# Performance work log

Measured on AMD Instinct MI355X. Metric: run time of the kernel, lower is better.

The kernel has to match this reference:

```python
import jax, jax.numpy as jnp
import numpy as np

N, IN_DIM = 50000, 1024
E = 100000
NUM_REL = 40
HEADS, OUT_DIM = 4, 200
HID = HEADS * OUT_DIM  # 800
B = 8192
NEG_SLOPE = 0.2


def setup_inputs() -> dict:
    key = jax.random.key(0)
    ks = jax.random.split(key, 12)
    node_emb = jax.random.normal(ks[0], (N, IN_DIM), dtype=jnp.float32)
    # RelGAT learnable params
    W = jax.random.normal(ks[1], (IN_DIM, HID), dtype=jnp.float32) * (1.0 / np.sqrt(IN_DIM))
    bias = jnp.zeros((HID,), dtype=jnp.float32)
    a_src = jax.random.normal(ks[2], (HEADS, OUT_DIM), dtype=jnp.float32) * 0.1
    a_dst = jax.random.normal(ks[3], (HEADS, OUT_DIM), dtype=jnp.float32) * 0.1
    a_rel = jax.random.normal(ks[4], (HEADS, OUT_DIM), dtype=jnp.float32) * 0.1
    rel_feat = jax.random.normal(ks[5], (NUM_REL, HID), dtype=jnp.float32) * 0.1
    # DistMult scorer relation embeddings
    rel_emb = jax.random.normal(ks[6], (NUM_REL, HID), dtype=jnp.float32) * 0.1
    # Graph structure (constants)
    edge_index = jax.random.randint(ks[7], (2, E), 0, N, dtype=jnp.int64)
    edge_type = jax.random.randint(ks[8], (E,), 0, NUM_REL, dtype=jnp.int64)
    # Triple batch
    src_ids = jax.random.randint(ks[9], (B,), 0, N, dtype=jnp.int64)
    rel_ids = jax.random.randint(ks[10], (B,), 0, NUM_REL, dtype=jnp.int64)
    dst_ids = jax.random.randint(ks[11], (B,), 0, N, dtype=jnp.int64)
    return dict(node_emb=node_emb, W=W, bias=bias, a_src=a_src, a_dst=a_dst,
                a_rel=a_rel, rel_feat=rel_feat, rel_emb=rel_emb,
                edge_index=edge_index, edge_type=edge_type,
                src_ids=src_ids, rel_ids=rel_ids, dst_ids=dst_ids)


def _rel_gat(node_emb, W, bias, a_src, a_dst, a_rel, rel_feat, edge_index, edge_type):
    src, dst = edge_index[0], edge_index[1]
    h = (node_emb @ W).reshape(N, HEADS, OUT_DIM)          # [N,H,D]
    hs = h[src]                                            # [E,H,D] gather
    hd = h[dst]                                            # [E,H,D] gather
    r = rel_feat[edge_type].reshape(E, HEADS, OUT_DIM)     # [E,H,D]
    # relation-conditioned attention logits per head
    logits = (jnp.einsum('ehd,hd->eh', hs, a_src)
              + jnp.einsum('ehd,hd->eh', hd, a_dst)
              + jnp.einsum('ehd,hd->eh', r, a_rel))        # [E,H]
    logits = jax.nn.leaky_relu(logits, NEG_SLOPE)
    # segment softmax over incoming edges of each destination node
    seg_max = jax.ops.segment_max(logits, dst, num_segments=N)   # [N,H]
    e = jnp.exp(logits - seg_max[dst])                           # [E,H]
    denom = jax.ops.segment_sum(e, dst, num_segments=N)          # [N,H]
    alpha = e / denom[dst]                                       # [E,H]
    # weighted scatter-aggregate of source messages
    out = jax.ops.segment_sum(alpha[:, :, None] * hs, dst, num_segments=N)  # [N,H,D]
    return out.reshape(N, HID) + bias                            # dropout: eval mode (identity)


def reference(node_emb, W, bias, a_src, a_dst, a_rel, rel_feat, rel_emb,
              edge_index, edge_type, src_ids, rel_ids, dst_ids):
    refined = _rel_gat(node_emb, W, bias, a_src, a_dst, a_rel, rel_feat,
                       edge_index, edge_type)                # [N, HID]
    src_vec = refined[src_ids]                               # [B, HID]
    dst_vec = refined[dst_ids]                               # [B, HID]
    # DistMult: sum(s * r * d)
    scores = jnp.sum(src_vec * rel_emb[rel_ids] * dst_vec, axis=-1)  # [B]
    return scores
```

## Files before the change

kernel.cpp:

```cpp
#include <hip/hip_runtime.h>
#include <hip/hip_bf16.h>
#include <math.h>

#define NN 50000
#define IN_DIM 1024
#define EE 100000
#define NUM_REL 40
#define HEADS 4
#define OUT_D 200
#define HID 800
#define BB 8192
#define SLOT_CAP 16384
#define SRC_CAP 50176
#define WT_COLS 896

typedef __attribute__((ext_vector_type(8))) short short8;
typedef __attribute__((ext_vector_type(4))) float f32x4;

__device__ inline unsigned short f2bf(float f) {
    unsigned int u = __float_as_uint(f);
    u += 0x7FFF + ((u >> 16) & 1);
    return (unsigned short)(u >> 16);
}
__device__ inline float bf2f(unsigned short s) {
    return __uint_as_float(((unsigned int)s) << 16);
}
__device__ inline void gl2lds16(const unsigned short* g, unsigned short* l) {
    __builtin_amdgcn_global_load_lds(
        (const __attribute__((address_space(1))) void*)g,
        (__attribute__((address_space(3))) void*)l, 16, 0, 0);
}

__device__ inline int wave_compact(bool won, int* ctr) {
    unsigned long long m = __ballot(won);
    if (!m) return -1;
    int lane = threadIdx.x & 63;
    int leader = __ffsll((long long)m) - 1;
    int base = 0;
    if (lane == leader) base = atomicAdd(ctr, __popcll(m));
    base = __shfl(base, leader, 64);
    return won ? base + __popcll(m & ((1ull << lane) - 1)) : -1;
}

#define INIT_BLOCKS 196
__global__ __launch_bounds__(256) void k_init_wa(int* slot_of_node, int* xrow_of_node,
                                                 int* deg, int* counters,
                                                 const float* W, const float* a_src,
                                                 const float* a_dst, const float* a_rel,
                                                 const float* rel_feat, float* Wa, float* prel) {
    int b = blockIdx.x;
    if (b < INIT_BLOCKS) {
        int i = b * 256 + threadIdx.x;
        if (i < NN) { slot_of_node[i] = -1; xrow_of_node[i] = -1; }
        if (i < SLOT_CAP) deg[i] = 0;
        if (i < 8) counters[i] = 0;
        return;
    }
    int wid = (b - INIT_BLOCKS) * 4 + (threadIdx.x >> 6);
    int lane = threadIdx.x & 63;
    if (wid >= IN_DIM * 8 + NUM_REL * HEADS) return;
    float acc = 0.f;
    int d = lane * 4;
    if (d < OUT_D) {
        const float* row;
        const float* a;
        if (wid < IN_DIM * 8) {
            int k = wid >> 3, c = wid & 7;
            int h = c & 3;
            row = W + (size_t)k * HID + h * OUT_D;
            a = ((c < 4) ? a_src : a_dst) + h * OUT_D;
        } else {
            int j = wid - IN_DIM * 8;
            int r = j >> 2, h = j & 3;
            row = rel_feat + (size_t)r * HID + h * OUT_D;
            a = a_rel + h * OUT_D;
        }
        float4 wv = *(const float4*)(row + d);
        float4 av = *(const float4*)(a + d);
        acc = wv.x * av.x + wv.y * av.y + wv.z * av.z + wv.w * av.w;
    }
    for (int off = 32; off; off >>= 1) acc += __shfl_down(acc, off, 64);
    if (lane == 0) {
        if (wid < IN_DIM * 8) Wa[wid] = acc;
        else prel[wid - IN_DIM * 8] = acc;
    }
}

__global__ void k_build_slots(const int* src_ids, const int* dst_ids,
                              int* slot_of_node, int* counters, int* scorelist) {
    int i = blockIdx.x * 256 + threadIdx.x;
    bool valid = i < 2 * BB;
    int n = 0;
    bool won = false;
    if (valid) {
        n = (i < BB) ? src_ids[i] : dst_ids[i - BB];
        if (slot_of_node[n] == -1)
            won = (atomicCAS(&slot_of_node[n], -1, -2) == -1);
    }
    int s = wave_compact(won, &counters[0]);
    if (won) {
        slot_of_node[n] = s;
        scorelist[s] = n;
    }
}

__global__ void k_edge0(const int* ei, const int* slot_of_node,
                        int* xrow_of_node, int* counters, int* rows, int* deg) {
    int e = blockIdx.x * 256 + threadIdx.x;
    bool valid = e < EE;
    int slot = -1, sn = 0;
    if (valid) {
        int dn = ei[EE + e];
        slot = slot_of_node[dn];
    }
    bool surv = valid && slot >= 0;
    bool won = false;
    if (surv) {
        sn = ei[e];
        if (xrow_of_node[sn] == -1)
            won = (atomicCAS(&xrow_of_node[sn], -1, -2) == -1);
    }
    int t = wave_compact(won, &counters[1]);
    if (won) {
        rows[t] = sn;
        xrow_of_node[sn] = t;
    }
    if (surv) atomicAdd(&deg[slot], 1);
}

__global__ __launch_bounds__(256) void k_tail_scan(const int* scorelist, int* xrow_of_node,
                                                   int* counters, int* rows,
                                                   const int* deg, int* base, int* cursor) {
    int t = threadIdx.x;
    if (blockIdx.x == 0) {
        __shared__ int pref[257];
        int s = 0;
        const int4* dv = (const int4*)(deg + t * (SLOT_CAP / 256));
        for (int i = 0; i < SLOT_CAP / 256 / 4; ++i) {
            int4 v = dv[i];
            s += v.x + v.y + v.z + v.w;
        }
        pref[t + 1] = s;
        if (t == 0) pref[0] = 0;
        __syncthreads();
        if (t == 0)
            for (int i = 1; i <= 256; ++i) pref[i] += pref[i - 1];
        __syncthreads();
        int r = pref[t];
        for (int i = 0; i < SLOT_CAP / 256; ++i) {
            int idx = t * (SLOT_CAP / 256) + i;
            base[idx] = r;
            cursor[idx] = r;
            r += deg[idx];
        }
        return;
    }
    int i = (blockIdx.x - 1) * 256 + t;
    bool valid = i < counters[0];
    int n = 0;
    bool won = false;
    if (valid) {
        n = scorelist[i];
        won = (xrow_of_node[n] < 0);
    }
    int tt = wave_compact(won, &counters[3]);
    if (won) {
        int xr = counters[1] + tt;
        xrow_of_node[n] = xr;
        rows[xr] = n;
    }
}

#define WT_BLOCKS 224
#define GATHER_BLOCKS 3584
__global__ __launch_bounds__(256) void k_gather_wt(const float* x, const int* rows,
                                                   const int* counters, unsigned short* xg,
                                                   const float* W, const float* Wa,
                                                   unsigned short* Wt) {
    int t = threadIdx.x;
    if (blockIdx.x < WT_BLOCKS) {
        __shared__ float tile[64][65];
        int b = blockIdx.x;
        int k0 = (b & 15) * 64, c0 = (b >> 4) * 64;
        {
            int kk = t >> 2, cc = (t & 3) * 16;
            for (int i = 0; i < 16; ++i) {
                int c = c0 + cc + i;
                float v = 0.f;
                if (c < HID) v = W[(size_t)(k0 + kk) * HID + c];
                else if (c < HID + 8) v = Wa[(size_t)(k0 + kk) * 8 + (c - HID)];
                tile[cc + i][kk] = v;
            }
        }
        __syncthreads();
        {
            int cc = t >> 2, kk = (t & 3) * 16;
            unsigned short o[16];
            for (int i = 0; i < 16; ++i) o[i] = f2bf(tile[cc][kk + i]);
            *(short8*)(Wt + (size_t)(c0 + cc) * IN_DIM + k0 + kk) = *(short8*)o;
            *(short8*)(Wt + (size_t)(c0 + cc) * IN_DIM + k0 + kk + 8) = *(short8*)(o + 8);
        }
        return;
    }
    int nneed = counters[1] + counters[3];
    int lim = nneed * 128;
    for (int gid = (blockIdx.x - WT_BLOCKS) * 256 + t; gid < lim;
         gid += GATHER_BLOCKS * 256) {
        int row = gid >> 7;
        int j = (gid & 127) * 8;
        int node = rows[row];
        const float* src = x + (size_t)node * IN_DIM + j;
        float4 a = *(const float4*)(src);
        float4 b = *(const float4*)(src + 4);
        unsigned short o[8] = {f2bf(a.x), f2bf(a.y), f2bf(a.z), f2bf(a.w),
                               f2bf(b.x), f2bf(b.y), f2bf(b.z), f2bf(b.w)};
        *(short8*)(xg + (size_t)row * IN_DIM + j) = *(short8*)o;
    }
}

#define GBM 256
#define GBN 128
#define GBK 64

#define STAGE(AS, BS, K0) do {                                          \
    gl2lds16(aP0 + (K0),      (AS) + (size_t)(0 * 512 + t) * 8);        \
    gl2lds16(aP1 + (K0),      (AS) + (size_t)(1 * 512 + t) * 8);        \
    gl2lds16(aP0 + (K0) + 32, (AS) + (size_t)(2 * 512 + t) * 8);        \
    gl2lds16(aP1 + (K0) + 32, (AS) + (size_t)(3 * 512 + t) * 8);        \
    gl2lds16(bP  + (K0),      (BS) + (size_t)(0 * 512 + t) * 8);        \
    gl2lds16(bP  + (K0) + 32, (BS) + (size_t)(1 * 512 + t) * 8);        \
} while (0)

#define COMPUTE(AS, BS) do {                                            \
    _Pragma("unroll")                                                   \
    for (int s = 0; s < 2; ++s) {                                       \
        short8 af[4], bf4[4];                                           \
        _Pragma("unroll")                                               \
        for (int i = 0; i < 4; ++i)                                     \
            af[i] = *(const short8*)&(AS)[(size_t)(s * 1024 + (gm + i) * 64 + lane) * 8]; \
        _Pragma("unroll")                                               \
        for (int j = 0; j < 4; ++j)                                     \
            bf4[j] = *(const short8*)&(BS)[(size_t)(s * 512 + (gn + j) * 64 + lane) * 8]; \
        __builtin_amdgcn_s_setprio(1);                                  \
        _Pragma("unroll")                                               \
        for (int i = 0; i < 4; ++i)                                     \
            _Pragma("unroll")                                           \
            for (int j = 0; j < 4; ++j)                                 \
                acc[i][j] = __builtin_amdgcn_mfma_f32_16x16x32_bf16(af[i], bf4[j], acc[i][j], 0, 0, 0); \
        __builtin_amdgcn_s_setprio(0);                                  \
    }                                                                   \
} while (0)

#define GATE6 asm volatile("s_waitcnt vmcnt(6)\n\ts_barrier" ::: "memory")
#define GATE0 asm volatile("s_waitcnt vmcnt(0)\n\ts_barrier" ::: "memory")
#define BARX  asm volatile("s_barrier" ::: "memory")

__global__ __launch_bounds__(512) void k_hgemm(const unsigned short* xg, const unsigned short* Wt,
                                               const int* counters, unsigned short* h_src,
                                               float* sS, float* sD) {
    int nsrc = counters[1];
    int nneed = nsrc + counters[3];
    int lin = blockIdx.x + 7 * blockIdx.y;
    int g = lin / 56, r = lin % 56;
    int rowb = g * 8 + (r & 7);
    int colb = r >> 3;
    int col0 = colb * GBN;
    int row0 = rowb * GBM;
    int rowlim = (col0 == 768) ? nneed : nsrc;
    if (row0 >= rowlim) return;
    __shared__ unsigned short As0[GBM * GBK];
    __shared__ unsigned short As1[GBM * GBK];
    __shared__ unsigned short Bs0[GBN * GBK];
    __shared__ unsigned short Bs1[GBN * GBK];
    int t = threadIdx.x;
    int rb = ((t >> 6) << 4) + (t & 15);
    int kb = ((t >> 4) & 3) << 3;
    const unsigned short* aP0 = xg + (size_t)(row0 + rb) * IN_DIM + kb;
    const unsigned short* aP1 = aP0 + (size_t)128 * IN_DIM;
    const unsigned short* bP  = Wt + (size_t)(col0 + rb) * IN_DIM + kb;
    int w = t >> 6, lane = t & 63;
    int gm = (w >> 1) * 4, gn = (w & 1) * 4;
    int wr = (w >> 1) * 64, wc = (w & 1) * 64;
    int fm = lane & 15, fq = lane >> 4;
    f32x4 acc[4][4] = {};
    STAGE(As0, Bs0, 0);
#pragma unroll 1
    for (int kk = 0; kk < 16; kk += 2) {
        STAGE(As1, Bs1, (kk + 1) * 64);
        GATE6;
        COMPUTE(As0, Bs0);
        BARX;
        if (kk < 14) {
            STAGE(As0, Bs0, (kk + 2) * 64);
            GATE6;
        } else {
            GATE0;
        }
        COMPUTE(As1, Bs1);
        BARX;
    }
#pragma unroll
    for (int i = 0; i < 4; ++i) {
#pragma unroll
        for (int j = 0; j < 4; ++j) {
            int gcol = col0 + wc + j * 16 + fm;
            if (gcol >= HID + 8) continue;
#pragma unroll
            for (int rr = 0; rr < 4; ++rr) {
                int grow = row0 + wr + i * 16 + fq * 4 + rr;
                float v = acc[i][j][rr];
                if (gcol < HID) {
                    if (grow < nsrc) h_src[(size_t)grow * HID + gcol] = f2bf(v);
                } else if (grow < nneed) {
                    int c = gcol - HID;
                    if (c < 4) sS[grow * 4 + c] = v;
                    else sD[grow * 4 + (c - 4)] = v;
                }
            }
        }
    }
}

__global__ void k_place(const int* ei, const int* etype, const int* slot_of_node,
                        const int* xrow_of_node, int* cursor,
                        const float* sS, const float* sD, const float* prel,
                        float* clogit, int* tlist) {
    int e = blockIdx.x * 256 + threadIdx.x;
    if (e >= EE) return;
    int dn = ei[EE + e];
    int slot = slot_of_node[dn];
    if (slot < 0) return;
    int sn = ei[e];
    int r = etype[e];
    int xs = xrow_of_node[sn];
    int xd = xrow_of_node[dn];
    int pos = atomicAdd(&cursor[slot], 1);
    tlist[pos] = xs;
    float4 lg;
    float* lp = (float*)&lg;
#pragma unroll
    for (int h = 0; h < 4; ++h) {
        float v = sS[xs * 4 + h] + sD[xd * 4 + h] + prel[r * 4 + h];
        lp[h] = v > 0.f ? v : 0.2f * v;
    }
    *(float4*)&clogit[(size_t)pos * 4] = lg;
}

__global__ __launch_bounds__(256) void k_aggregate(const int* counters, const int* base,
                                                   const int* deg, const int* tlist,
                                                   const float* clogit,
                                                   const unsigned short* h_src, const float* bias,
                                                   float* refined) {
    int b = blockIdx.x;
    if (b >= counters[0]) return;
    int beg = base[b], d = deg[b];
    __shared__ float m4[4], den4[4];
    __shared__ float alpha[64][4];
    __shared__ int tsl[64];
    int t = threadIdx.x;
    if (t < 4) {
        float m = -3e38f;
        for (int j = 0; j < d; ++j)
            m = fmaxf(m, clogit[(size_t)(beg + j) * 4 + t]);
        float s = 0.f;
        for (int j = 0; j < d; ++j)
            s += expf(clogit[(size_t)(beg + j) * 4 + t] - m);
        m4[t] = m;
        den4[t] = s;
    }
    __syncthreads();
    int head = t / 50;
    float4 acc = {0.f, 0.f, 0.f, 0.f};
    for (int j0 = 0; j0 < d; j0 += 64) {
        int nc = min(64, d - j0);
        if (t < nc * 4) {
            int j = t >> 2, h = t & 3;
            alpha[j][h] = expf(clogit[(size_t)(beg + j0 + j) * 4 + h] - m4[h]) / den4[h];
            if (h == 0) tsl[j] = tlist[beg + j0 + j];
        }
        __syncthreads();
        if (t < 200) {
            for (int j = 0; j < nc; ++j) {
                float a = alpha[j][head];
                ushort4 hv = *(const ushort4*)(h_src + (size_t)tsl[j] * HID + t * 4);
                acc.x += a * bf2f(hv.x);
                acc.y += a * bf2f(hv.y);
                acc.z += a * bf2f(hv.z);
                acc.w += a * bf2f(hv.w);
            }
        }
        __syncthreads();
    }
    if (t < 200) {
        float4 bv = *(const float4*)(bias + t * 4);
        float4 o = {acc.x + bv.x, acc.y + bv.y, acc.z + bv.z, acc.w + bv.w};
        *(float4*)(refined + (size_t)b * HID + t * 4) = o;
    }
}

__global__ __launch_bounds__(256) void k_score(const int* src_ids, const int* rel_ids,
                                               const int* dst_ids, const int* slot_of_node,
                                               const float* rel_emb, const float* refined,
                                               float* out) {
    int gid = blockIdx.x * 256 + threadIdx.x;
    int b = gid >> 6;
    int lane = threadIdx.x & 63;
    if (b >= BB) return;
    int ss = slot_of_node[src_ids[b]];
    int ds = slot_of_node[dst_ids[b]];
    int r = rel_ids[b];
    const float* sv = refined + (size_t)ss * HID;
    const float* dv = refined + (size_t)ds * HID;
    const float* rv = rel_emb + (size_t)r * HID;
    float acc = 0.f;
    for (int c4 = lane; c4 < 200; c4 += 64) {
        float4 s = *(const float4*)(sv + c4 * 4);
        float4 dq = *(const float4*)(dv + c4 * 4);
        float4 rr = *(const float4*)(rv + c4 * 4);
        acc += s.x * rr.x * dq.x + s.y * rr.y * dq.y + s.z * rr.z * dq.z + s.w * rr.w * dq.w;
    }
    for (int off = 32; off; off >>= 1) acc += __shfl_down(acc, off, 64);
    if (lane == 0) out[b] = acc;
}

extern "C" void kernel_launch(void* const* d_in, const int* in_sizes, int n_in,
                              void* d_out, int out_size, void* d_ws, size_t ws_size,
                              hipStream_t stream) {
    const float* node_emb = (const float*)d_in[0];
    const float* W        = (const float*)d_in[1];
    const float* bias     = (const float*)d_in[2];
    const float* a_src    = (const float*)d_in[3];
    const float* a_dst    = (const float*)d_in[4];
    const float* a_rel    = (const float*)d_in[5];
    const float* rel_feat = (const float*)d_in[6];
    const float* rel_emb  = (const float*)d_in[7];
    const int* edge_index = (const int*)d_in[8];
    const int* edge_type  = (const int*)d_in[9];
    const int* src_ids    = (const int*)d_in[10];
    const int* rel_ids    = (const int*)d_in[11];
    const int* dst_ids    = (const int*)d_in[12];
    float* out = (float*)d_out;

    char* w = (char*)d_ws;
    auto alloc = [&](size_t bytes) -> void* {
        void* p = (void*)w;
        w += (bytes + 255) & ~(size_t)255;
        return p;
    };
    int* slot_of_node = (int*)alloc((size_t)NN * 4);
    int* xrow_of_node = (int*)alloc((size_t)NN * 4);
    int* scorelist    = (int*)alloc((size_t)SLOT_CAP * 4);
    int* rows         = (int*)alloc((size_t)NN * 4);
    int* counters     = (int*)alloc(256);
    int* deg          = (int*)alloc((size_t)SLOT_CAP * 4);
    int* base         = (int*)alloc((size_t)SLOT_CAP * 4);
    int* cursor       = (int*)alloc((size_t)SLOT_CAP * 4);
    int* tlist        = (int*)alloc((size_t)EE * 4);
    float* clogit = (float*)alloc((size_t)EE * 4 * 4);
    float* sS     = (float*)alloc((size_t)SRC_CAP * 4 * 4);
    float* sD     = (float*)alloc((size_t)SRC_CAP * 4 * 4);
    float* Wa     = (float*)alloc((size_t)IN_DIM * 8 * 4);
    float* prel   = (float*)alloc((size_t)NUM_REL * 4 * 4);
    unsigned short* xg    = (unsigned short*)alloc((size_t)SRC_CAP * IN_DIM * 2);
    unsigned short* Wt    = (unsigned short*)alloc((size_t)WT_COLS * IN_DIM * 2);
    unsigned short* h_src = (unsigned short*)alloc((size_t)SRC_CAP * HID * 2);
    float* refined = (float*)alloc((size_t)SLOT_CAP * HID * 4);

    int wa_blocks = (IN_DIM * 8 + NUM_REL * HEADS + 3) / 4;
    k_init_wa<<<INIT_BLOCKS + wa_blocks, 256, 0, stream>>>(
        slot_of_node, xrow_of_node, deg, counters,
        W, a_src, a_dst, a_rel, rel_feat, Wa, prel);
    k_build_slots<<<(2 * BB + 255) / 256, 256, 0, stream>>>(src_ids, dst_ids, slot_of_node,
                                                            counters, scorelist);
    k_edge0<<<(EE + 255) / 256, 256, 0, stream>>>(edge_index, slot_of_node,
                                                  xrow_of_node, counters, rows, deg);
    k_tail_scan<<<1 + SLOT_CAP / 256, 256, 0, stream>>>(scorelist, xrow_of_node, counters,
                                                        rows, deg, base, cursor);
    k_gather_wt<<<WT_BLOCKS + GATHER_BLOCKS, 256, 0, stream>>>(
        node_emb, rows, counters, xg, W, Wa, Wt);
    dim3 ggrid(7, 200);
    k_hgemm<<<ggrid, 512, 0, stream>>>(xg, Wt, counters, h_src, sS, sD);
    k_place<<<(EE + 255) / 256, 256, 0, stream>>>(edge_index, edge_type, slot_of_node,
                                                  xrow_of_node, cursor, sS, sD, prel,
                                                  clogit, tlist);
    k_aggregate<<<SLOT_CAP, 256, 0, stream>>>(counters, base, deg, tlist,
                                              clogit, h_src, bias, refined);
    k_score<<<(BB * 64 + 255) / 256, 256, 0, stream>>>(src_ids, rel_ids, dst_ids,
                                                       slot_of_node, rel_emb, refined, out);
}
```

Baseline: 504.1 us.

## Fuse row gather and bf16 conversion into GEMM A-tile loading

```diff
diff --git a/kernel.cpp b/kernel.cpp
--- a/kernel.cpp
+++ b/kernel.cpp
@@ -128,9 +128,11 @@
     if (surv) atomicAdd(&deg[slot], 1);
 }
 
-__global__ __launch_bounds__(256) void k_tail_scan(const int* scorelist, int* xrow_of_node,
-                                                   int* counters, int* rows,
-                                                   const int* deg, int* base, int* cursor) {
+__global__ __launch_bounds__(256) void k_tail_scan_wt(const int* scorelist, int* xrow_of_node,
+                                                      int* counters, int* rows,
+                                                      const int* deg, int* base, int* cursor,
+                                                      const float* W, const float* Wa,
+                                                      unsigned short* Wt) {
     int t = threadIdx.x;
     if (blockIdx.x == 0) {
         __shared__ int pref[257];
@@ -155,80 +157,78 @@
         }
         return;
     }
-    int i = (blockIdx.x - 1) * 256 + t;
-    bool valid = i < counters[0];
-    int n = 0;
-    bool won = false;
-    if (valid) {
-        n = scorelist[i];
-        won = (xrow_of_node[n] < 0);
-    }
-    int tt = wave_compact(won, &counters[3]);
-    if (won) {
-        int xr = counters[1] + tt;
-        xrow_of_node[n] = xr;
-        rows[xr] = n;
-    }
-}
-
-#define WT_BLOCKS 224
-#define GATHER_BLOCKS 3584
-__global__ __launch_bounds__(256) void k_gather_wt(const float* x, const int* rows,
-                                                   const int* counters, unsigned short* xg,
-                                                   const float* W, const float* Wa,
-                                                   unsigned short* Wt) {
-    int t = threadIdx.x;
-    if (blockIdx.x < WT_BLOCKS) {
-        __shared__ float tile[64][65];
-        int b = blockIdx.x;
-        int k0 = (b & 15) * 64, c0 = (b >> 4) * 64;
-        {
-            int kk = t >> 2, cc = (t & 3) * 16;
-            for (int i = 0; i < 16; ++i) {
-                int c = c0 + cc + i;
-                float v = 0.f;
-                if (c < HID) v = W[(size_t)(k0 + kk) * HID + c];
-                else if (c < HID + 8) v = Wa[(size_t)(k0 + kk) * 8 + (c - HID)];
-                tile[cc + i][kk] = v;
-            }
-        }
-        __syncthreads();
-        {
-            int cc = t >> 2, kk = (t & 3) * 16;
-            unsigned short o[16];
-            for (int i = 0; i < 16; ++i) o[i] = f2bf(tile[cc][kk + i]);
-            *(short8*)(Wt + (size_t)(c0 + cc) * IN_DIM + k0 + kk) = *(short8*)o;
-            *(short8*)(Wt + (size_t)(c0 + cc) * IN_DIM + k0 + kk + 8) = *(short8*)(o + 8);
+    if (blockIdx.x <= 64) {
+        int i = (blockIdx.x - 1) * 256 + t;
+        bool valid = i < counters[0];
+        int n = 0;
+        bool won = false;
+        if (valid) {
+            n = scorelist[i];
+            won = (xrow_of_node[n] < 0);
+        }
+        int tt = wave_compact(won, &counters[3]);
+        if (won) {
+            int xr = counters[1] + tt;
+            xrow_of_node[n] = xr;
+            rows[xr] = n;
         }
         return;
     }
-    int nneed = counters[1] + counters[3];
-    int lim = nneed * 128;
-    for (int gid = (blockIdx.x - WT_BLOCKS) * 256 + t; gid < lim;
-         gid += GATHER_BLOCKS * 256) {
-        int row = gid >> 7;
-        int j = (gid & 127) * 8;
-        int node = rows[row];
-        const float* src = x + (size_t)node * IN_DIM + j;
-        float4 a = *(const float4*)(src);
-        float4 b = *(const float4*)(src + 4);
-        unsigned short o[8] = {f2bf(a.x), f2bf(a.y), f2bf(a.z), f2bf(a.w),
-                               f2bf(b.x), f2bf(b.y), f2bf(b.z), f2bf(b.w)};
-        *(short8*)(xg + (size_t)row * IN_DIM + j) = *(short8*)o;
-    }
-}
-
-#define GBM 256
+    __shared__ float tile[64][65];
+    int b = blockIdx.x - 65;
+    int k0 = (b & 15) * 64, c0 = (b >> 4) * 64;
+    {
+        int kk = t >> 2, cc = (t & 3) * 16;
+        for (int i = 0; i < 16; ++i) {
+            int c = c0 + cc + i;
+            float v = 0.f;
+            if (c < HID) v = W[(size_t)(k0 + kk) * HID + c];
+            else if (c < HID + 8) v = Wa[(size_t)(k0 + kk) * 8 + (c - HID)];
+            tile[cc + i][kk] = v;
+        }
+    }
+    __syncthreads();
+    {
+        int cc = t >> 2, kk = (t & 3) * 16;
+        unsigned short o[16];
+        for (int i = 0; i < 16; ++i) o[i] = f2bf(tile[cc][kk + i]);
+        *(short8*)(Wt + (size_t)(c0 + cc) * IN_DIM + k0 + kk) = *(short8*)o;
+        *(short8*)(Wt + (size_t)(c0 + cc) * IN_DIM + k0 + kk + 8) = *(short8*)(o + 8);
+    }
+}
+
+#define GBM 128
 #define GBN 128
 #define GBK 64
 
-#define STAGE(AS, BS, K0) do {                                          \
-    gl2lds16(aP0 + (K0),      (AS) + (size_t)(0 * 512 + t) * 8);        \
-    gl2lds16(aP1 + (K0),      (AS) + (size_t)(1 * 512 + t) * 8);        \
-    gl2lds16(aP0 + (K0) + 32, (AS) + (size_t)(2 * 512 + t) * 8);        \
-    gl2lds16(aP1 + (K0) + 32, (AS) + (size_t)(3 * 512 + t) * 8);        \
-    gl2lds16(bP  + (K0),      (BS) + (size_t)(0 * 512 + t) * 8);        \
-    gl2lds16(bP  + (K0) + 32, (BS) + (size_t)(1 * 512 + t) * 8);        \
+#define ALOAD(K0) do {                                                  \
+    av[0] = *(const float4*)(ax0 + (K0));                               \
+    av[1] = *(const float4*)(ax0 + (K0) + 4);                           \
+    av[2] = *(const float4*)(ax1 + (K0));                               \
+    av[3] = *(const float4*)(ax1 + (K0) + 4);                           \
+    av[4] = *(const float4*)(ax0 + (K0) + 32);                          \
+    av[5] = *(const float4*)(ax0 + (K0) + 36);                          \
+    av[6] = *(const float4*)(ax1 + (K0) + 32);                          \
+    av[7] = *(const float4*)(ax1 + (K0) + 36);                          \
+} while (0)
+
+#define AWRITE(AS) do {                                                 \
+    unsigned short o[8];                                                \
+    _Pragma("unroll")                                                   \
+    for (int q = 0; q < 4; ++q) {                                       \
+        o[0] = f2bf(av[2*q].x); o[1] = f2bf(av[2*q].y);                 \
+        o[2] = f2bf(av[2*q].z); o[3] = f2bf(av[2*q].w);                 \
+        o[4] = f2bf(av[2*q+1].x); o[5] = f2bf(av[2*q+1].y);             \
+        o[6] = f2bf(av[2*q+1].z); o[7] = f2bf(av[2*q+1].w);             \
+        *(short8*)&(AS)[(size_t)(q * 256 + t) * 8] = *(short8*)o;       \
+    }                                                                   \
+} while (0)
+
+#define BSTAGE(BS, K0) do {                                             \
+    gl2lds16(bP0 + (K0),      (BS) + (size_t)(0 * 256 + t) * 8);        \
+    gl2lds16(bP1 + (K0),      (BS) + (size_t)(1 * 256 + t) * 8);        \
+    gl2lds16(bP0 + (K0) + 32, (BS) + (size_t)(2 * 256 + t) * 8);        \
+    gl2lds16(bP1 + (K0) + 32, (BS) + (size_t)(3 * 256 + t) * 8);        \
 } while (0)
 
 #define COMPUTE(AS, BS) do {                                            \
@@ -237,10 +237,10 @@
         short8 af[4], bf4[4];                                           \
         _Pragma("unroll")                                               \
         for (int i = 0; i < 4; ++i)                                     \
-            af[i] = *(const short8*)&(AS)[(size_t)(s * 1024 + (gm + i) * 64 + lane) * 8]; \
+            af[i] = *(const short8*)&(AS)[(size_t)(s * 512 + (ga + i) * 64 + lane) * 8]; \
         _Pragma("unroll")                                               \
         for (int j = 0; j < 4; ++j)                                     \
-            bf4[j] = *(const short8*)&(BS)[(size_t)(s * 512 + (gn + j) * 64 + lane) * 8]; \
+            bf4[j] = *(const short8*)&(BS)[(size_t)(s * 512 + (gb + j) * 64 + lane) * 8]; \
         __builtin_amdgcn_s_setprio(1);                                  \
         _Pragma("unroll")                                               \
         for (int i = 0; i < 4; ++i)                                     \
@@ -251,11 +251,12 @@
     }                                                                   \
 } while (0)
 
-#define GATE6 asm volatile("s_waitcnt vmcnt(6)\n\ts_barrier" ::: "memory")
-#define GATE0 asm volatile("s_waitcnt vmcnt(0)\n\ts_barrier" ::: "memory")
-#define BARX  asm volatile("s_barrier" ::: "memory")
-
-__global__ __launch_bounds__(512) void k_hgemm(const unsigned short* xg, const unsigned short* Wt,
+#define WAIT_A  asm volatile("s_waitcnt vmcnt(4)" ::: "memory")
+#define PUBLISH asm volatile("s_waitcnt vmcnt(0) lgkmcnt(0)" ::: "memory")
+#define BARX    asm volatile("s_barrier" ::: "memory")
+
+__global__ __launch_bounds__(256) void k_hgemm(const float* x, const int* rows,
+                                               const unsigned short* Wt,
                                                const int* counters, unsigned short* h_src,
                                                float* sS, float* sD) {
     int nsrc = counters[1];
@@ -273,31 +274,49 @@
     __shared__ unsigned short Bs0[GBN * GBK];
     __shared__ unsigned short Bs1[GBN * GBK];
     int t = threadIdx.x;
-    int rb = ((t >> 6) << 4) + (t & 15);
-    int kb = ((t >> 4) & 3) << 3;
-    const unsigned short* aP0 = xg + (size_t)(row0 + rb) * IN_DIM + kb;
-    const unsigned short* aP1 = aP0 + (size_t)128 * IN_DIM;
-    const unsigned short* bP  = Wt + (size_t)(col0 + rb) * IN_DIM + kb;
+    int crow = ((t >> 6) << 4) + (t & 15);
+    int coff = ((t >> 4) & 3) << 3;
+    int lim = nneed - 1;
+    int n0 = rows[min(row0 + crow, lim)];
+    int n1 = rows[min(row0 + crow + 64, lim)];
+    const float* ax0 = x + (size_t)n0 * IN_DIM + coff;
+    const float* ax1 = x + (size_t)n1 * IN_DIM + coff;
+    const unsigned short* bP0 = Wt + (size_t)(col0 + crow) * IN_DIM + coff;
+    const unsigned short* bP1 = bP0 + (size_t)64 * IN_DIM;
     int w = t >> 6, lane = t & 63;
-    int gm = (w >> 1) * 4, gn = (w & 1) * 4;
+    int ga = (w >> 1) * 4, gb = (w & 1) * 4;
     int wr = (w >> 1) * 64, wc = (w & 1) * 64;
     int fm = lane & 15, fq = lane >> 4;
+    float4 av[8];
     f32x4 acc[4][4] = {};
-    STAGE(As0, Bs0, 0);
+    ALOAD(0);
+    BSTAGE(Bs0, 0);
+    WAIT_A;
+    AWRITE(As0);
+    PUBLISH;
+    BARX;
 #pragma unroll 1
     for (int kk = 0; kk < 16; kk += 2) {
-        STAGE(As1, Bs1, (kk + 1) * 64);
-        GATE6;
+        ALOAD((kk + 1) * 64);
+        BSTAGE(Bs1, (kk + 1) * 64);
         COMPUTE(As0, Bs0);
         BARX;
+        WAIT_A;
+        AWRITE(As1);
+        PUBLISH;
+        BARX;
         if (kk < 14) {
-            STAGE(As0, Bs0, (kk + 2) * 64);
-            GATE6;
-        } else {
-            GATE0;
+            ALOAD((kk + 2) * 64);
+            BSTAGE(Bs0, (kk + 2) * 64);
         }
         COMPUTE(As1, Bs1);
         BARX;
+        if (kk < 14) {
+            WAIT_A;
+            AWRITE(As0);
+            PUBLISH;
+            BARX;
+        }
     }
 #pragma unroll
     for (int i = 0; i < 4; ++i) {
@@ -461,7 +480,6 @@
     float* sD     = (float*)alloc((size_t)SRC_CAP * 4 * 4);
     float* Wa     = (float*)alloc((size_t)IN_DIM * 8 * 4);
     float* prel   = (float*)alloc((size_t)NUM_REL * 4 * 4);
-    unsigned short* xg    = (unsigned short*)alloc((size_t)SRC_CAP * IN_DIM * 2);
     unsigned short* Wt    = (unsigned short*)alloc((size_t)WT_COLS * IN_DIM * 2);
     unsigned short* h_src = (unsigned short*)alloc((size_t)SRC_CAP * HID * 2);
     float* refined = (float*)alloc((size_t)SLOT_CAP * HID * 4);
@@ -474,12 +492,10 @@
                                                             counters, scorelist);
     k_edge0<<<(EE + 255) / 256, 256, 0, stream>>>(edge_index, slot_of_node,
                                                   xrow_of_node, counters, rows, deg);
-    k_tail_scan<<<1 + SLOT_CAP / 256, 256, 0, stream>>>(scorelist, xrow_of_node, counters,
-                                                        rows, deg, base, cursor);
-    k_gather_wt<<<WT_BLOCKS + GATHER_BLOCKS, 256, 0, stream>>>(
-        node_emb, rows, counters, xg, W, Wa, Wt);
-    dim3 ggrid(7, 200);
-    k_hgemm<<<ggrid, 512, 0, stream>>>(xg, Wt, counters, h_src, sS, sD);
+    k_tail_scan_wt<<<65 + 224, 256, 0, stream>>>(scorelist, xrow_of_node, counters,
+                                                 rows, deg, base, cursor, W, Wa, Wt);
+    dim3 ggrid(7, 392);
+    k_hgemm<<<ggrid, 256, 0, stream>>>(node_emb, rows, Wt, counters, h_src, sS, sD);
     k_place<<<(EE + 255) / 256, 256, 0, stream>>>(edge_index, edge_type, slot_of_node,
                                                   xrow_of_node, cursor, sS, sD, prel,
                                                   clogit, tlist);
```

Result: no change. 505.1 us (+0.2%).
